# Kernel tuning notes

Hardware: AMD Instinct MI355X
Metric: run time of the kernel (lower is better)

## Reference

```python
import jax, jax.numpy as jnp
import numpy as np

N_NODES = 50000
N_EDGES = 800000
D_IN = 256
D_OUT = 128


def setup_inputs() -> dict:
    key = jax.random.key(0)
    k1, k2, k3 = jax.random.split(key, 3)
    x = jax.random.normal(k1, (N_NODES, D_IN), dtype=jnp.float32)
    edge_index = jax.random.randint(k2, (2, N_EDGES), 0, N_NODES, dtype=jnp.int64)
    W = jax.random.normal(k3, (D_IN, D_OUT), dtype=jnp.float32) / np.sqrt(D_IN)
    b = jnp.zeros((D_OUT,), dtype=jnp.float32)
    prelu_a = jnp.full((D_OUT,), 0.25, dtype=jnp.float32)  # PyTorch PReLU default init
    return {"x": x, "edge_index": edge_index, "W": W, "b": b, "prelu_a": prelu_a}


def reference(x, edge_index, W, b, prelu_a):
    N = x.shape[0]
    # GCNConv default: add self-loops, symmetric deg^{-1/2} normalization
    self_loops = jnp.arange(N, dtype=edge_index.dtype)
    src = jnp.concatenate([edge_index[0], self_loops])  # message source j
    dst = jnp.concatenate([edge_index[1], self_loops])  # aggregation target i
    deg = jax.ops.segment_sum(jnp.ones_like(dst, dtype=x.dtype), dst, num_segments=N)
    dinv = jnp.where(deg > 0, jax.lax.rsqrt(deg), 0.0)
    norm = dinv[src] * dinv[dst]  # [E+N]
    h = x @ W  # [N, D_OUT] linear transform before aggregation
    msg = h[src] * norm[:, None]  # gather + scale
    out = jax.ops.segment_sum(msg, dst, num_segments=N) + b  # scatter-add + bias
    # per-channel PReLU
    return jnp.where(out > 0, out, prelu_a * out)
```

## Files before the change

### kernel.cpp

```cpp
#include <hip/hip_runtime.h>

#define N_NODES 50000
#define N_EDGES 800000
#define D_IN    256
#define D_OUT   128
#define ELL_S   64
#define GEMM_BLKS ((N_NODES + 127) / 128)
#define NBINS   196
#define BCAP    5120
#define PART_BLKS 391
#define EPB     2048
#define CNT_N   (NBINS * 256)

typedef __attribute__((ext_vector_type(8))) short short8;
typedef __attribute__((ext_vector_type(4))) float floatx4;

__device__ __forceinline__ unsigned short f2bf(float f) {
    unsigned int u = __float_as_uint(f);
    unsigned int r = (u + 0x7fffu + ((u >> 16) & 1u)) >> 16;
    return (unsigned short)r;
}
__device__ __forceinline__ unsigned int pack2(float a, float b) {
    return (unsigned int)f2bf(a) | ((unsigned int)f2bf(b) << 16);
}
__device__ __forceinline__ float bfl(unsigned int u) { return __uint_as_float(u << 16); }
__device__ __forceinline__ float bfh(unsigned int u) { return __uint_as_float(u & 0xffff0000u); }

__global__ __launch_bounds__(256) void prep_kernel(const unsigned int* __restrict__ e,
                                                   int* __restrict__ is64,
                                                   const float* __restrict__ W,
                                                   unsigned short* __restrict__ bf,
                                                   int* __restrict__ binCur) {
    int bid = blockIdx.x;
    int tid = threadIdx.x;
    if (bid == 0) {
        __shared__ int found32;
        if (tid == 0) found32 = 0;
        __syncthreads();
        for (int i = tid; i < 2048; i += 256)
            if (e[2 * i + 1] != 0u) found32 = 1;
        __syncthreads();
        if (tid == 0) *is64 = (found32 ? 0 : 1);
    } else if (bid <= 16) {
        int g = (bid - 1) * 256 + tid;
        int lane = g & 63;
        int kc   = (g >> 6) & 7;
        int ct   = g >> 9;
        int n  = ct * 16 + (lane & 15);
        int kb = kc * 32 + ((lane >> 4) & 3) * 8;
        unsigned int p[4];
#pragma unroll
        for (int jj = 0; jj < 4; jj++) {
            float a = W[(size_t)(kb + 2 * jj + 0) * D_OUT + n];
            float b = W[(size_t)(kb + 2 * jj + 1) * D_OUT + n];
            p[jj] = pack2(a, b);
        }
        *(uint4*)&bf[(size_t)g * 8] = make_uint4(p[0], p[1], p[2], p[3]);
    } else {
        if (tid < NBINS) binCur[tid] = 0;
    }
}

__global__ __launch_bounds__(256) void fused_kernel(const float* __restrict__ x,
                                                    const unsigned short* __restrict__ bf,
                                                    unsigned short* __restrict__ h,
                                                    const void* __restrict__ ei,
                                                    const int* __restrict__ is64p,
                                                    int* __restrict__ binCur,
                                                    int* __restrict__ packed) {
    __shared__ unsigned short As[128][40];
    __shared__ int hist[NBINS];
    __shared__ int curs[NBINS];
    int tid = threadIdx.x;

    if (blockIdx.x >= GEMM_BLKS) {
        int sb = blockIdx.x - GEMM_BLKS;
        for (int t = tid; t < NBINS; t += 256) hist[t] = 0;
        __syncthreads();
        int is64 = *is64p;
        int ebase = sb * EPB + tid;
        int sv[8], bn[8], dl[8], lr[8];
        if (is64) {
            const long long* p = (const long long*)ei;
#pragma unroll
            for (int i = 0; i < 8; i++) {
                int e = ebase + i * 256;
                if (e < N_EDGES) {
                    sv[i] = (int)p[e];
                    int d = (int)p[N_EDGES + e];
                    bn[i] = d >> 8; dl[i] = d & 255;
                } else bn[i] = -1;
            }
        } else {
            const int* p = (const int*)ei;
#pragma unroll
            for (int i = 0; i < 8; i++) {
                int e = ebase + i * 256;
                if (e < N_EDGES) {
                    sv[i] = p[e];
                    int d = p[N_EDGES + e];
                    bn[i] = d >> 8; dl[i] = d & 255;
                } else bn[i] = -1;
            }
        }
#pragma unroll
        for (int i = 0; i < 8; i++)
            if (bn[i] >= 0) lr[i] = atomicAdd(&hist[bn[i]], 1);
        __syncthreads();
        for (int t = tid; t < NBINS; t += 256) {
            int hc = hist[t];
            curs[t] = hc ? atomicAdd(&binCur[t], hc) : 0;
        }
        __syncthreads();
#pragma unroll
        for (int i = 0; i < 8; i++) {
            if (bn[i] >= 0) {
                int pos = curs[bn[i]] + lr[i];
                if (pos < BCAP)
                    packed[bn[i] * BCAP + pos] = sv[i] | (dl[i] << 24);
            }
        }
        return;
    }

    int row0 = blockIdx.x * 128;
    int w    = tid >> 6;
    int lane = tid & 63;
    int quad = lane >> 4;
    int l15  = lane & 15;

    floatx4 acc[2][8];
#pragma unroll
    for (int i = 0; i < 2; i++)
#pragma unroll
        for (int j = 0; j < 8; j++) acc[i][j] = (floatx4){0.f, 0.f, 0.f, 0.f};

    int srow  = tid >> 1;
    int shalf = (tid & 1) * 16;
    const float* xrow = x + (size_t)(row0 + srow) * D_IN;
    bool svalid = (row0 + srow) < N_NODES;

    for (int k0 = 0; k0 < D_IN; k0 += 32) {
        uint4 p0 = make_uint4(0, 0, 0, 0), p1 = make_uint4(0, 0, 0, 0);
        if (svalid) {
            const float* src = xrow + k0 + shalf;
            float4 f0 = *(const float4*)(src + 0);
            float4 f1 = *(const float4*)(src + 4);
            float4 f2 = *(const float4*)(src + 8);
            float4 f3 = *(const float4*)(src + 12);
            p0 = make_uint4(pack2(f0.x, f0.y), pack2(f0.z, f0.w),
                            pack2(f1.x, f1.y), pack2(f1.z, f1.w));
            p1 = make_uint4(pack2(f2.x, f2.y), pack2(f2.z, f2.w),
                            pack2(f3.x, f3.y), pack2(f3.z, f3.w));
        }
        __syncthreads();
        *(uint4*)&As[srow][shalf + 0] = p0;
        *(uint4*)&As[srow][shalf + 8] = p1;
        __syncthreads();

        short8 a0 = *(const short8*)&As[w * 32 + l15][quad * 8];
        short8 a1 = *(const short8*)&As[w * 32 + 16 + l15][quad * 8];
        int kc = k0 >> 5;
#pragma unroll
        for (int ct = 0; ct < 8; ct++) {
            short8 b = *(const short8*)&bf[(size_t)(((ct * 8 + kc) * 64 + lane)) * 8];
            acc[0][ct] = __builtin_amdgcn_mfma_f32_16x16x32_bf16(a0, b, acc[0][ct], 0, 0, 0);
            acc[1][ct] = __builtin_amdgcn_mfma_f32_16x16x32_bf16(a1, b, acc[1][ct], 0, 0, 0);
        }
    }

#pragma unroll
    for (int rt = 0; rt < 2; rt++) {
        int grow0 = row0 + w * 32 + rt * 16 + quad * 4;
#pragma unroll
        for (int r = 0; r < 4; r++) {
            int grow = grow0 + r;
            if (grow < N_NODES) {
#pragma unroll
                for (int ct = 0; ct < 8; ct++) {
                    h[(size_t)grow * D_OUT + ct * 16 + l15] = f2bf(acc[rt][ct][r]);
                }
            }
        }
    }
}

__global__ __launch_bounds__(256) void ell_kernel(const int* __restrict__ packed,
                                                  const int* __restrict__ binCur,
                                                  int* __restrict__ cnt,
                                                  int* __restrict__ bucket) {
    __shared__ int c256[256];
    int j = blockIdx.x, tid = threadIdx.x;
    c256[tid] = 0;
    __syncthreads();
    int m = binCur[j];
    if (m > BCAP) m = BCAP;
    const int* seg = packed + j * BCAP;
    for (int i = tid; i < m; i += 256) {
        int rec = seg[i];
        int dl  = ((unsigned int)rec) >> 24;
        int s   = rec & 0xFFFFFF;
        int pos = atomicAdd(&c256[dl], 1);
        if (pos < ELL_S) bucket[(size_t)((j << 8) + dl) * ELL_S + pos] = s;
    }
    __syncthreads();
    int d = (j << 8) + tid;
    if (d < N_NODES) cnt[d] = c256[tid];
}

#define GACC(U, F)                                      \
    a0 += bfl(U.x) * (F); a1 += bfh(U.x) * (F);         \
    a2 += bfl(U.y) * (F); a3 += bfh(U.y) * (F);         \
    a4 += bfl(U.z) * (F); a5 += bfh(U.z) * (F);         \
    a6 += bfl(U.w) * (F); a7 += bfh(U.w) * (F);

#define GBODY(SS, WW, KB)                                                         \
    {                                                                             \
        int lim = wave_max - (KB);                                                \
        if (lim > 16) lim = 16;                                                   \
        for (int k = 0; k < lim; k += 4) {                                        \
            int   s0 = __shfl((SS), gk + k + 0), s1 = __shfl((SS), gk + k + 1);   \
            int   s2 = __shfl((SS), gk + k + 2), s3 = __shfl((SS), gk + k + 3);   \
            float f0 = __shfl((WW), gk + k + 0), f1 = __shfl((WW), gk + k + 1);   \
            float f2 = __shfl((WW), gk + k + 2), f3 = __shfl((WW), gk + k + 3);   \
            uint4 u0 = *(const uint4*)(h + (size_t)s0 * D_OUT + co);              \
            uint4 u1 = *(const uint4*)(h + (size_t)s1 * D_OUT + co);              \
            uint4 u2 = *(const uint4*)(h + (size_t)s2 * D_OUT + co);              \
            uint4 u3 = *(const uint4*)(h + (size_t)s3 * D_OUT + co);              \
            GACC(u0, f0); GACC(u1, f1); GACC(u2, f2); GACC(u3, f3);               \
        }                                                                         \
    }

__global__ __launch_bounds__(256) void gather_kernel(
    const unsigned short* __restrict__ h, const int* __restrict__ cnt,
    const int* __restrict__ bucket, const float* __restrict__ bias,
    const float* __restrict__ pa, float* __restrict__ out) {
    int wave = (int)((blockIdx.x * blockDim.x + threadIdx.x) >> 6);
    int lane = threadIdx.x & 63;
    int g  = lane >> 4;
    int l  = lane & 15;
    int gk = g << 4;
    int d  = wave * 4 + g;
    if (wave >= N_NODES / 4) return;

    int nraw = cnt[d];
    int n = nraw < ELL_S ? nraw : ELL_S;
    float di = rsqrtf((float)(nraw + 1));

    int co = l * 8;

    uint4 us = *(const uint4*)(h + (size_t)d * D_OUT + co);
    float sl = di * di;
    float a0 = bfl(us.x) * sl, a1 = bfh(us.x) * sl;
    float a2 = bfl(us.y) * sl, a3 = bfh(us.y) * sl;
    float a4 = bfl(us.z) * sl, a5 = bfh(us.z) * sl;
    float a6 = bfl(us.w) * sl, a7 = bfh(us.w) * sl;

    int db = d * ELL_S;
    int   s0v = 0,   s1v = 0,   s2v = 0,   s3v = 0;
    float w0v = 0.f, w1v = 0.f, w2v = 0.f, w3v = 0.f;
    if (l      < n) { s0v = bucket[db + l];      w0v = rsqrtf((float)(cnt[s0v] + 1)) * di; }
    if (l + 16 < n) { s1v = bucket[db + l + 16]; w1v = rsqrtf((float)(cnt[s1v] + 1)) * di; }
    if (l + 32 < n) { s2v = bucket[db + l + 32]; w2v = rsqrtf((float)(cnt[s2v] + 1)) * di; }
    if (l + 48 < n) { s3v = bucket[db + l + 48]; w3v = rsqrtf((float)(cnt[s3v] + 1)) * di; }

    int wave_max = n;
    { int t = __shfl_xor(wave_max, 16); wave_max = t > wave_max ? t : wave_max; }
    { int t = __shfl_xor(wave_max, 32); wave_max = t > wave_max ? t : wave_max; }

    if (wave_max > 0)  GBODY(s0v, w0v, 0)
    if (wave_max > 16) GBODY(s1v, w1v, 16)
    if (wave_max > 32) GBODY(s2v, w2v, 32)
    if (wave_max > 48) GBODY(s3v, w3v, 48)

    int c = l * 8;
    float4 b0 = *(const float4*)&bias[c];
    float4 b1 = *(const float4*)&bias[c + 4];
    float4 p0 = *(const float4*)&pa[c];
    float4 p1 = *(const float4*)&pa[c + 4];
    float4 o0, o1;
    o0.x = a0 + b0.x; o0.y = a1 + b0.y; o0.z = a2 + b0.z; o0.w = a3 + b0.w;
    o1.x = a4 + b1.x; o1.y = a5 + b1.y; o1.z = a6 + b1.z; o1.w = a7 + b1.w;
    o0.x = o0.x > 0.f ? o0.x : p0.x * o0.x;
    o0.y = o0.y > 0.f ? o0.y : p0.y * o0.y;
    o0.z = o0.z > 0.f ? o0.z : p0.z * o0.z;
    o0.w = o0.w > 0.f ? o0.w : p0.w * o0.w;
    o1.x = o1.x > 0.f ? o1.x : p1.x * o1.x;
    o1.y = o1.y > 0.f ? o1.y : p1.y * o1.y;
    o1.z = o1.z > 0.f ? o1.z : p1.z * o1.z;
    o1.w = o1.w > 0.f ? o1.w : p1.w * o1.w;
    *(float4*)&out[(size_t)d * D_OUT + c]     = o0;
    *(float4*)&out[(size_t)d * D_OUT + c + 4] = o1;
}

extern "C" void kernel_launch(void* const* d_in, const int* in_sizes, int n_in,
                              void* d_out, int out_size, void* d_ws, size_t ws_size,
                              hipStream_t stream) {
    const float* x  = (const float*)d_in[0];
    const void*  ei = d_in[1];
    const float* W  = (const float*)d_in[2];
    const float* b  = (const float*)d_in[3];
    const float* pa = (const float*)d_in[4];
    float* out = (float*)d_out;

    char* w = (char*)d_ws;
    int*   is64   = (int*)w;    w += 256;
    int*   binCur = (int*)w;    w += 1024;
    int*   cnt    = (int*)w;    w += (size_t)CNT_N * 4;
    unsigned short* bfrag = (unsigned short*)w; w += 8 * 8 * 64 * 8 * 2;
    int*   packed = (int*)w;    w += (size_t)NBINS * BCAP * 4;
    int*   bucket = (int*)w;    w += (size_t)N_NODES * ELL_S * 4;
    unsigned short* h = (unsigned short*)w; w += (size_t)N_NODES * D_OUT * 2;

    prep_kernel<<<18, 256, 0, stream>>>((const unsigned int*)ei, is64, W, bfrag, binCur);
    fused_kernel<<<GEMM_BLKS + PART_BLKS, 256, 0, stream>>>(x, bfrag, h, ei, is64, binCur, packed);
    ell_kernel<<<NBINS, 256, 0, stream>>>(packed, binCur, cnt, bucket);
    gather_kernel<<<(N_NODES / 4 * 64 + 255) / 256, 256, 0, stream>>>(h, cnt, bucket, b, pa, out);
}
```

Measured before the change: 164.9 us.

## Drop prep kernel; use per-block bin slots instead of global atomic cursors

Removes the separate prep kernel. Each partition block now detects the index width itself, and each GEMM block packs W into bf16 fragments in its own LDS. Partition blocks write edges into fixed per-(block,bin) slots of capacity 40 and record their counts, so the global atomic cursor and its zeroing are gone. The ELL kernel then walks all 391 block slots per bin, with each thread handling one block's segment serially. This saves a launch and the global atomics, but every GEMM block redoes the W repack and uses more LDS. Any edges beyond 40 per block-bin are silently dropped.

```diff
diff --git a/kernel.cpp b/kernel.cpp
--- a/kernel.cpp
+++ b/kernel.cpp
@@ -5,12 +5,11 @@
 #define D_IN    256
 #define D_OUT   128
 #define ELL_S   64
-#define GEMM_BLKS ((N_NODES + 127) / 128)
+#define PART_BLKS 391
+#define GEMM_BLKS 391
 #define NBINS   196
-#define BCAP    5120
-#define PART_BLKS 391
 #define EPB     2048
-#define CNT_N   (NBINS * 256)
+#define CAPB    40
 
 typedef __attribute__((ext_vector_type(8))) short short8;
 typedef __attribute__((ext_vector_type(4))) float floatx4;
@@ -26,58 +25,31 @@
 __device__ __forceinline__ float bfl(unsigned int u) { return __uint_as_float(u << 16); }
 __device__ __forceinline__ float bfh(unsigned int u) { return __uint_as_float(u & 0xffff0000u); }
 
-__global__ __launch_bounds__(256) void prep_kernel(const unsigned int* __restrict__ e,
-                                                   int* __restrict__ is64,
-                                                   const float* __restrict__ W,
-                                                   unsigned short* __restrict__ bf,
-                                                   int* __restrict__ binCur) {
-    int bid = blockIdx.x;
-    int tid = threadIdx.x;
-    if (bid == 0) {
-        __shared__ int found32;
+__global__ __launch_bounds__(256) void fused_kernel(const float* __restrict__ x,
+                                                    const float* __restrict__ W,
+                                                    const void* __restrict__ ei,
+                                                    int* __restrict__ packed,
+                                                    int* __restrict__ blkBinCnt,
+                                                    unsigned short* __restrict__ h) {
+    __shared__ unsigned short As[128][40];
+    __shared__ unsigned short bLds[4096 * 8];
+    __shared__ int hist[NBINS];
+    __shared__ int found32;
+    const int bid = blockIdx.x;
+    const int tid = threadIdx.x;
+
+    if (bid < PART_BLKS) {
+        int sb = bid;
+        if (tid < NBINS) hist[tid] = 0;
         if (tid == 0) found32 = 0;
         __syncthreads();
-        for (int i = tid; i < 2048; i += 256)
-            if (e[2 * i + 1] != 0u) found32 = 1;
-        __syncthreads();
-        if (tid == 0) *is64 = (found32 ? 0 : 1);
-    } else if (bid <= 16) {
-        int g = (bid - 1) * 256 + tid;
-        int lane = g & 63;
-        int kc   = (g >> 6) & 7;
-        int ct   = g >> 9;
-        int n  = ct * 16 + (lane & 15);
-        int kb = kc * 32 + ((lane >> 4) & 3) * 8;
-        unsigned int p[4];
-#pragma unroll
-        for (int jj = 0; jj < 4; jj++) {
-            float a = W[(size_t)(kb + 2 * jj + 0) * D_OUT + n];
-            float b = W[(size_t)(kb + 2 * jj + 1) * D_OUT + n];
-            p[jj] = pack2(a, b);
-        }
-        *(uint4*)&bf[(size_t)g * 8] = make_uint4(p[0], p[1], p[2], p[3]);
-    } else {
-        if (tid < NBINS) binCur[tid] = 0;
-    }
-}
-
-__global__ __launch_bounds__(256) void fused_kernel(const float* __restrict__ x,
-                                                    const unsigned short* __restrict__ bf,
-                                                    unsigned short* __restrict__ h,
-                                                    const void* __restrict__ ei,
-                                                    const int* __restrict__ is64p,
-                                                    int* __restrict__ binCur,
-                                                    int* __restrict__ packed) {
-    __shared__ unsigned short As[128][40];
-    __shared__ int hist[NBINS];
-    __shared__ int curs[NBINS];
-    int tid = threadIdx.x;
-
-    if (blockIdx.x >= GEMM_BLKS) {
-        int sb = blockIdx.x - GEMM_BLKS;
-        for (int t = tid; t < NBINS; t += 256) hist[t] = 0;
-        __syncthreads();
-        int is64 = *is64p;
+        {
+            const unsigned int* e32 = (const unsigned int*)ei;
+            if (e32[2 * tid + 1] != 0u) atomicOr(&found32, 1);
+        }
+        __syncthreads();
+        int is64 = !found32;
+
         int ebase = sb * EPB + tid;
         int sv[8], bn[8], dl[8], lr[8];
         if (is64) {
@@ -106,24 +78,36 @@
 #pragma unroll
         for (int i = 0; i < 8; i++)
             if (bn[i] >= 0) lr[i] = atomicAdd(&hist[bn[i]], 1);
-        __syncthreads();
-        for (int t = tid; t < NBINS; t += 256) {
-            int hc = hist[t];
-            curs[t] = hc ? atomicAdd(&binCur[t], hc) : 0;
-        }
-        __syncthreads();
 #pragma unroll
         for (int i = 0; i < 8; i++) {
-            if (bn[i] >= 0) {
-                int pos = curs[bn[i]] + lr[i];
-                if (pos < BCAP)
-                    packed[bn[i] * BCAP + pos] = sv[i] | (dl[i] << 24);
-            }
-        }
+            if (bn[i] >= 0 && lr[i] < CAPB)
+                packed[((size_t)sb * NBINS + bn[i]) * CAPB + lr[i]] = sv[i] | (dl[i] << 24);
+        }
+        __syncthreads();
+        for (int t = tid; t < NBINS; t += 256)
+            blkBinCnt[sb * NBINS + t] = hist[t];
         return;
     }
 
-    int row0 = blockIdx.x * 128;
+#pragma unroll
+    for (int seg = 0; seg < 16; seg++) {
+        int g = seg * 256 + tid;
+        int gl = g & 63;
+        int kc = (g >> 6) & 7;
+        int ct = g >> 9;
+        int n  = ct * 16 + (gl & 15);
+        int kb = kc * 32 + ((gl >> 4) & 3) * 8;
+        unsigned int p[4];
+#pragma unroll
+        for (int jj = 0; jj < 4; jj++) {
+            float a = W[(size_t)(kb + 2 * jj + 0) * D_OUT + n];
+            float b = W[(size_t)(kb + 2 * jj + 1) * D_OUT + n];
+            p[jj] = pack2(a, b);
+        }
+        *(uint4*)&bLds[(size_t)g * 8] = make_uint4(p[0], p[1], p[2], p[3]);
+    }
+
+    int row0 = (bid - PART_BLKS) * 128;
     int w    = tid >> 6;
     int lane = tid & 63;
     int quad = lane >> 4;
@@ -163,7 +147,7 @@
         int kc = k0 >> 5;
 #pragma unroll
         for (int ct = 0; ct < 8; ct++) {
-            short8 b = *(const short8*)&bf[(size_t)(((ct * 8 + kc) * 64 + lane)) * 8];
+            short8 b = *(const short8*)&bLds[(size_t)(((ct * 8 + kc) * 64 + lane)) * 8];
             acc[0][ct] = __builtin_amdgcn_mfma_f32_16x16x32_bf16(a0, b, acc[0][ct], 0, 0, 0);
             acc[1][ct] = __builtin_amdgcn_mfma_f32_16x16x32_bf16(a1, b, acc[1][ct], 0, 0, 0);
         }
@@ -186,22 +170,24 @@
 }
 
 __global__ __launch_bounds__(256) void ell_kernel(const int* __restrict__ packed,
-                                                  const int* __restrict__ binCur,
+                                                  const int* __restrict__ blkBinCnt,
                                                   int* __restrict__ cnt,
                                                   int* __restrict__ bucket) {
     __shared__ int c256[256];
     int j = blockIdx.x, tid = threadIdx.x;
     c256[tid] = 0;
     __syncthreads();
-    int m = binCur[j];
-    if (m > BCAP) m = BCAP;
-    const int* seg = packed + j * BCAP;
-    for (int i = tid; i < m; i += 256) {
-        int rec = seg[i];
-        int dl  = ((unsigned int)rec) >> 24;
-        int s   = rec & 0xFFFFFF;
-        int pos = atomicAdd(&c256[dl], 1);
-        if (pos < ELL_S) bucket[(size_t)((j << 8) + dl) * ELL_S + pos] = s;
+    for (int sb = tid; sb < PART_BLKS; sb += 256) {
+        int c = blkBinCnt[sb * NBINS + j];
+        if (c > CAPB) c = CAPB;
+        const int* seg = packed + ((size_t)sb * NBINS + j) * CAPB;
+        for (int r = 0; r < c; ++r) {
+            int rec = seg[r];
+            int dl  = ((unsigned int)rec) >> 24;
+            int s   = rec & 0xFFFFFF;
+            int pos = atomicAdd(&c256[dl], 1);
+            if (pos < ELL_S) bucket[(size_t)((j << 8) + dl) * ELL_S + pos] = s;
+        }
     }
     __syncthreads();
     int d = (j << 8) + tid;
@@ -304,16 +290,13 @@
     float* out = (float*)d_out;
 
     char* w = (char*)d_ws;
-    int*   is64   = (int*)w;    w += 256;
-    int*   binCur = (int*)w;    w += 1024;
-    int*   cnt    = (int*)w;    w += (size_t)CNT_N * 4;
-    unsigned short* bfrag = (unsigned short*)w; w += 8 * 8 * 64 * 8 * 2;
-    int*   packed = (int*)w;    w += (size_t)NBINS * BCAP * 4;
+    int*   packed = (int*)w;    w += (size_t)PART_BLKS * NBINS * CAPB * 4;
+    int*   bbc    = (int*)w;    w += (size_t)PART_BLKS * NBINS * 4;
+    int*   cnt    = (int*)w;    w += (size_t)NBINS * 256 * 4;
     int*   bucket = (int*)w;    w += (size_t)N_NODES * ELL_S * 4;
     unsigned short* h = (unsigned short*)w; w += (size_t)N_NODES * D_OUT * 2;
 
-    prep_kernel<<<18, 256, 0, stream>>>((const unsigned int*)ei, is64, W, bfrag, binCur);
-    fused_kernel<<<GEMM_BLKS + PART_BLKS, 256, 0, stream>>>(x, bfrag, h, ei, is64, binCur, packed);
-    ell_kernel<<<NBINS, 256, 0, stream>>>(packed, binCur, cnt, bucket);
+    fused_kernel<<<PART_BLKS + GEMM_BLKS, 256, 0, stream>>>(x, W, ei, packed, bbc, h);
+    ell_kernel<<<NBINS, 256, 0, stream>>>(packed, bbc, cnt, bucket);
     gather_kernel<<<(N_NODES / 4 * 64 + 255) / 256, 256, 0, stream>>>(h, cnt, bucket, b, pa, out);
 }
```

After: 170.0 us. 1.03x slower.
